# Optimization experiments

Hardware: AMD Instinct MI355X
Metric: run time of the kernel (lower is better)

Reference implementation:

```python
import jax, jax.numpy as jnp
import numpy as np

N_NODES = 100000
D_FEAT = 32
N_EDGES = 1600000


def setup_inputs() -> dict:
    key = jax.random.key(0)
    k1, k2, k3 = jax.random.split(key, 3)
    h = jax.random.normal(k1, (N_NODES, D_FEAT), dtype=jnp.float32)
    src = jax.random.randint(k2, (N_EDGES,), 0, N_NODES, dtype=jnp.int64)
    dst = jax.random.randint(k3, (N_EDGES,), 0, N_NODES, dtype=jnp.int64)
    return {"h": h, "src": src, "dst": dst}


def reference(h, src, dst):
    # u_dot_v: per-edge dot product of source and destination node features.
    # score[e] = sum_d h[src[e], d] * h[dst[e], d]  -> shape [E, 1] (DGL keeps a trailing dim)
    score = jnp.sum(h[src] * h[dst], axis=-1, keepdims=True)
    return score
```

## Files before the change

kernel.cpp:

```cpp
#include <hip/hip_runtime.h>


constexpr int D_FEAT = 32;

static __device__ __forceinline__ float bf_lo(unsigned u) {
    return __uint_as_float(u << 16);
}
static __device__ __forceinline__ float bf_hi(unsigned u) {
    return __uint_as_float(u & 0xffff0000u);
}
static __device__ __forceinline__ unsigned short f2bf_rne(float f) {
    unsigned u = __float_as_uint(f);
    u = (u + 0x7fffu + ((u >> 16) & 1u)) >> 16;
    return (unsigned short)u;
}

__global__ void __launch_bounds__(256) convert_h_bf16(
    const float4* __restrict__ h4, ushort4* __restrict__ hb4, int n4)
{
    int i = blockIdx.x * blockDim.x + threadIdx.x;
    const int stride = gridDim.x * blockDim.x;
    for (; i < n4; i += stride) {
        const float4 v = h4[i];
        ushort4 o;
        o.x = f2bf_rne(v.x);
        o.y = f2bf_rne(v.y);
        o.z = f2bf_rne(v.z);
        o.w = f2bf_rne(v.w);
        hb4[i] = o;
    }
}

__global__ void __launch_bounds__(256) edge_dot_bf16(
    const unsigned short* __restrict__ hb,
    const int* __restrict__ src,
    const int* __restrict__ dst,
    float* __restrict__ out,
    int n_edges)
{
    const int g = threadIdx.x & 3;
    const int group = (blockIdx.x * blockDim.x + threadIdx.x) >> 2;
    const int n_groups = (gridDim.x * blockDim.x) >> 2;

    for (int e = group; e < n_edges; e += n_groups) {
        const int s = src[e];
        const int d = dst[e];
        const uint4 a = reinterpret_cast<const uint4*>(hb + (size_t)s * D_FEAT)[g];
        const uint4 b = reinterpret_cast<const uint4*>(hb + (size_t)d * D_FEAT)[g];
        float acc;
        acc  = bf_lo(a.x) * bf_lo(b.x) + bf_hi(a.x) * bf_hi(b.x);
        acc += bf_lo(a.y) * bf_lo(b.y) + bf_hi(a.y) * bf_hi(b.y);
        acc += bf_lo(a.z) * bf_lo(b.z) + bf_hi(a.z) * bf_hi(b.z);
        acc += bf_lo(a.w) * bf_lo(b.w) + bf_hi(a.w) * bf_hi(b.w);
        acc += __shfl_xor(acc, 1);
        acc += __shfl_xor(acc, 2);
        if (g == 0) out[e] = acc;
    }
}

__global__ void __launch_bounds__(256) edge_dot_f32(
    const float* __restrict__ h,
    const int* __restrict__ src,
    const int* __restrict__ dst,
    float* __restrict__ out,
    int n_edges)
{
    const int g = threadIdx.x & 7;
    const int group = (blockIdx.x * blockDim.x + threadIdx.x) >> 3;
    const int n_groups = (gridDim.x * blockDim.x) >> 3;
    for (int e = group; e < n_edges; e += n_groups) {
        const int s = src[e];
        const int d = dst[e];
        const float4 a = reinterpret_cast<const float4*>(h + (size_t)s * D_FEAT)[g];
        const float4 b = reinterpret_cast<const float4*>(h + (size_t)d * D_FEAT)[g];
        float acc = a.x * b.x + a.y * b.y + a.z * b.z + a.w * b.w;
        acc += __shfl_xor(acc, 1);
        acc += __shfl_xor(acc, 2);
        acc += __shfl_xor(acc, 4);
        if (g == 0) out[e] = acc;
    }
}

extern "C" void kernel_launch(void* const* d_in, const int* in_sizes, int n_in,
                              void* d_out, int out_size, void* d_ws, size_t ws_size,
                              hipStream_t stream) {
    const float* h   = (const float*)d_in[0];
    const int*   src = (const int*)d_in[1];
    const int*   dst = (const int*)d_in[2];
    float*       out = (float*)d_out;
    const int n_h     = in_sizes[0];
    const int n_edges = in_sizes[1];

    const size_t need = (size_t)n_h * sizeof(unsigned short);
    if (ws_size >= need) {
        unsigned short* hb = (unsigned short*)d_ws;
        const int n4 = n_h / 4;
        convert_h_bf16<<<2048, 256, 0, stream>>>(
            (const float4*)h, (ushort4*)hb, n4);
        edge_dot_bf16<<<2048, 256, 0, stream>>>(hb, src, dst, out, n_edges);
    } else {
        edge_dot_f32<<<2048, 256, 0, stream>>>(h, src, dst, out, n_edges);
    }
}
```

Baseline: 41.53 us.

## Split bf16 feature table into two half-width planes processed in separate passes

The bf16 conversion now writes the node features as two planes, each holding 16 features per node, and the edge kernel runs twice, once per plane, with the second pass accumulating into the output. The goal is a smaller gather working set per pass so random row fetches stay in L2. In exchange, the src/dst indices are read twice, the output is read back and rewritten, and an extra kernel launch is added.

```diff
diff --git a/kernel.cpp b/kernel.cpp
--- a/kernel.cpp
+++ b/kernel.cpp
@@ -1,7 +1,14 @@
 #include <hip/hip_runtime.h>
 
 
-constexpr int D_FEAT = 32;
+constexpr int D_FEAT  = 32;
+constexpr int HALF_SH = 16;
+constexpr int GRID    = 2048;
+constexpr int BLOCK   = 256;
+
+typedef float          f32x4 __attribute__((ext_vector_type(4)));
+typedef unsigned int   u32x2 __attribute__((ext_vector_type(2)));
+typedef unsigned short u16x4 __attribute__((ext_vector_type(4)));
 
 static __device__ __forceinline__ float bf_lo(unsigned u) {
     return __uint_as_float(u << 16);
@@ -15,23 +22,30 @@
     return (unsigned short)u;
 }
 
-__global__ void __launch_bounds__(256) convert_h_bf16(
-    const float4* __restrict__ h4, ushort4* __restrict__ hb4, int n4)
+__global__ void __launch_bounds__(256) convert_h_planes(
+    const f32x4* __restrict__ h4,
+    unsigned short* __restrict__ hb0,
+    unsigned short* __restrict__ hb1,
+    int n4)
 {
     int i = blockIdx.x * blockDim.x + threadIdx.x;
     const int stride = gridDim.x * blockDim.x;
     for (; i < n4; i += stride) {
-        const float4 v = h4[i];
-        ushort4 o;
+        const f32x4 v = h4[i];
+        u16x4 o;
         o.x = f2bf_rne(v.x);
         o.y = f2bf_rne(v.y);
         o.z = f2bf_rne(v.z);
         o.w = f2bf_rne(v.w);
-        hb4[i] = o;
+        const int node = i >> 3;
+        const int q = i & 7;
+        unsigned short* base = (q < 4) ? hb0 : hb1;
+        *reinterpret_cast<u16x4*>(base + (size_t)node * HALF_SH + (q & 3) * 4) = o;
     }
 }
 
-__global__ void __launch_bounds__(256) edge_dot_bf16(
+template <bool ADD>
+__global__ void __launch_bounds__(256) edge_plane(
     const unsigned short* __restrict__ hb,
     const int* __restrict__ src,
     const int* __restrict__ dst,
@@ -40,21 +54,23 @@
 {
     const int g = threadIdx.x & 3;
     const int group = (blockIdx.x * blockDim.x + threadIdx.x) >> 2;
-    const int n_groups = (gridDim.x * blockDim.x) >> 2;
+    const int n_groups = (GRID * BLOCK) >> 2;
 
     for (int e = group; e < n_edges; e += n_groups) {
         const int s = src[e];
         const int d = dst[e];
-        const uint4 a = reinterpret_cast<const uint4*>(hb + (size_t)s * D_FEAT)[g];
-        const uint4 b = reinterpret_cast<const uint4*>(hb + (size_t)d * D_FEAT)[g];
-        float acc;
-        acc  = bf_lo(a.x) * bf_lo(b.x) + bf_hi(a.x) * bf_hi(b.x);
-        acc += bf_lo(a.y) * bf_lo(b.y) + bf_hi(a.y) * bf_hi(b.y);
-        acc += bf_lo(a.z) * bf_lo(b.z) + bf_hi(a.z) * bf_hi(b.z);
-        acc += bf_lo(a.w) * bf_lo(b.w) + bf_hi(a.w) * bf_hi(b.w);
+        const u32x2 a = *reinterpret_cast<const u32x2*>(
+            hb + (size_t)s * HALF_SH + g * 4);
+        const u32x2 b = *reinterpret_cast<const u32x2*>(
+            hb + (size_t)d * HALF_SH + g * 4);
+        float acc = bf_lo(a.x) * bf_lo(b.x) + bf_hi(a.x) * bf_hi(b.x)
+                  + bf_lo(a.y) * bf_lo(b.y) + bf_hi(a.y) * bf_hi(b.y);
         acc += __shfl_xor(acc, 1);
         acc += __shfl_xor(acc, 2);
-        if (g == 0) out[e] = acc;
+        if (g == 0) {
+            if (ADD) out[e] += acc;
+            else     out[e] = acc;
+        }
     }
 }
 
@@ -71,8 +87,8 @@
     for (int e = group; e < n_edges; e += n_groups) {
         const int s = src[e];
         const int d = dst[e];
-        const float4 a = reinterpret_cast<const float4*>(h + (size_t)s * D_FEAT)[g];
-        const float4 b = reinterpret_cast<const float4*>(h + (size_t)d * D_FEAT)[g];
+        const f32x4 a = reinterpret_cast<const f32x4*>(h + (size_t)s * D_FEAT)[g];
+        const f32x4 b = reinterpret_cast<const f32x4*>(h + (size_t)d * D_FEAT)[g];
         float acc = a.x * b.x + a.y * b.y + a.z * b.z + a.w * b.w;
         acc += __shfl_xor(acc, 1);
         acc += __shfl_xor(acc, 2);
@@ -90,14 +106,19 @@
     float*       out = (float*)d_out;
     const int n_h     = in_sizes[0];
     const int n_edges = in_sizes[1];
+    const int n_nodes = n_h / D_FEAT;
 
-    const size_t need = (size_t)n_h * sizeof(unsigned short);
-    if (ws_size >= need) {
-        unsigned short* hb = (unsigned short*)d_ws;
+    const size_t plane_bytes = (size_t)n_nodes * HALF_SH * sizeof(unsigned short);
+    if (ws_size >= 2 * plane_bytes) {
+        unsigned short* hb0 = (unsigned short*)d_ws;
+        unsigned short* hb1 = hb0 + (size_t)n_nodes * HALF_SH;
         const int n4 = n_h / 4;
-        convert_h_bf16<<<2048, 256, 0, stream>>>(
-            (const float4*)h, (ushort4*)hb, n4);
-        edge_dot_bf16<<<2048, 256, 0, stream>>>(hb, src, dst, out, n_edges);
+        convert_h_planes<<<GRID, BLOCK, 0, stream>>>(
+            (const f32x4*)h, hb0, hb1, n4);
+        edge_plane<false><<<GRID, BLOCK, 0, stream>>>(
+            hb0, src, dst, out, n_edges);
+        edge_plane<true><<<GRID, BLOCK, 0, stream>>>(
+            hb1, src, dst, out, n_edges);
     } else {
         edge_dot_f32<<<2048, 256, 0, stream>>>(h, src, dst, out, n_edges);
     }
```

Result: slower. 51.94 us (+25.1%).
